# Kernel tuning notes

Measured on AMD Instinct MI355X. Metric: run time of the kernel, lower is better.

## Reference

```python
import jax, jax.numpy as jnp
import numpy as np

B, T, D, S = 4, 8192, 512, 16

def setup_inputs() -> dict:
    key = jax.random.key(0)
    k1, k2, k3, k4, k5 = jax.random.split(key, 5)
    x = jax.random.normal(k1, (B, T, D), dtype=jnp.float32)
    # splat parameters as in __init__: centers ~ 0.02*randn, log_scales = 0
    centers = jax.random.normal(k2, (S, D), dtype=jnp.float32) * 0.02
    log_scales = jnp.zeros((S,), dtype=jnp.float32)
    # xavier-uniform linear weights (gain = 1/(1+layer_idx*0.1) = 1.0 for layer 0)
    limit = float(np.sqrt(6.0 / (D + D)))
    Wv = jax.random.uniform(k3, (D, D), minval=-limit, maxval=limit, dtype=jnp.float32)
    Wo = jax.random.uniform(k4, (D, D), minval=-limit, maxval=limit, dtype=jnp.float32)
    return {"x": x, "centers": centers, "log_scales": log_scales, "Wv": Wv, "Wo": Wo}

def reference(x, centers, log_scales, Wv, Wo):
    # scales clamped as in EnhancedAdaptiveSplat.get_scale
    scales = jnp.clip(jnp.exp(log_scales), 0.1, 2.0)           # [S]
    v = jnp.einsum('btd,ed->bte', x, Wv)                       # value projection [B,T,D]
    # squared distance token<->splat via expansion (no [B,T,S,D] intermediate)
    x2 = jnp.sum(x * x, axis=-1, keepdims=True)                # [B,T,1]
    c2 = jnp.sum(centers * centers, axis=-1)                   # [S]
    xc = jnp.einsum('btd,sd->bts', x, centers)                 # [B,T,S]
    d2 = x2 + c2 - 2.0 * xc                                    # [B,T,S]
    logits = -0.5 * d2 / (scales * scales)                     # gaussian kernel log-weights
    attn = jax.nn.softmax(logits, axis=-1)                     # normalize over splats [B,T,S]
    # tokens -> splats aggregation, then splats -> tokens distribution
    splat_states = jnp.einsum('bts,btd->bsd', attn, v)         # [B,S,D]
    out = jnp.einsum('bts,bsd->btd', attn, splat_states)       # [B,T,D]
    return jnp.einsum('btd,ed->bte', out, Wo)                  # output projection
```

## Files before the change

### kernel.cpp

```cpp
#include <hip/hip_runtime.h>
#include <hip/hip_bf16.h>
#include <math.h>

#define B_ 4
#define T_ 8192
#define D_ 512
#define S_ 16

#define CHUNK 64


typedef __attribute__((ext_vector_type(8))) short bf16x8;
typedef __attribute__((ext_vector_type(4))) float f32x4;

__device__ __forceinline__ float dot4(float4 a, float4 b) {
  return a.x * b.x + a.y * b.y + a.z * b.z + a.w * b.w;
}

__device__ __forceinline__ bf16x8 pack8(float4 a, float4 b) {
  union { __hip_bfloat162 h[4]; bf16x8 v; } u;
  u.h[0] = __float22bfloat162_rn(make_float2(a.x, a.y));
  u.h[1] = __float22bfloat162_rn(make_float2(a.z, a.w));
  u.h[2] = __float22bfloat162_rn(make_float2(b.x, b.y));
  u.h[3] = __float22bfloat162_rn(make_float2(b.z, b.w));
  return u.v;
}

__global__ __launch_bounds__(256, 2) void attn_ts_k(const float* __restrict__ x,
                                                    const float* __restrict__ centers,
                                                    const float* __restrict__ log_scales,
                                                    float* __restrict__ attn,
                                                    float* __restrict__ ts) {
  __shared__ __align__(16) float a_s[CHUNK][S_];
  __shared__ __align__(16) bf16x8 cf_s[16][64];
  __shared__ float c2_s[S_];
  const int tid = threadIdx.x;
  const int lane = tid & 63;
  const int w = tid >> 6;
  const int g = lane >> 4;
  const int n = lane & 15;
  const int b = blockIdx.x >> 7;
  const int t0 = (blockIdx.x & 127) * CHUNK;
  const int tw = t0 + (w << 4);

#pragma unroll
  for (int i = 0; i < 4; ++i) {
    int e = i * 256 + tid;
    int st = e >> 6;
    int ln = e & 63;
    int nn = ln & 15, gg = ln >> 4;
    const float* src = centers + nn * D_ + st * 32 + (gg << 3);
    float4 c0 = *(const float4*)(src);
    float4 c1 = *(const float4*)(src + 4);
    cf_s[st][ln] = pack8(c0, c1);
  }
  if (w == 0) {
    const float* crow = centers + n * D_ + (g << 7);
    float c2p = 0.f;
#pragma unroll
    for (int k = 0; k < 32; ++k) {
      float4 cv = *(const float4*)(crow + (k << 2));
      c2p += dot4(cv, cv);
    }
    c2p += __shfl_xor(c2p, 16, 64);
    c2p += __shfl_xor(c2p, 32, 64);
    if (lane < S_) c2_s[lane] = c2p;
  }
  __syncthreads();

  {
    const float sc = fminf(fmaxf(__expf(log_scales[n]), 0.1f), 2.0f);
    const float inv2 = 0.5f / (sc * sc);
    const bool uni =
        (__ballot(sc == __shfl(sc, 0, 64)) == 0xFFFFFFFFFFFFFFFFull);

    const float* xrow = x + ((size_t)b * T_ + tw + n) * D_ + (g << 3);
    f32x4 acc = {0.f, 0.f, 0.f, 0.f};
    float x2p = 0.f;

    float4 pb0[4], pb1[4];
#pragma unroll
    for (int i = 0; i < 4; ++i) {
      pb0[i] = *(const float4*)(xrow + i * 32);
      pb1[i] = *(const float4*)(xrow + i * 32 + 4);
    }

    if (uni) {
#pragma unroll
      for (int st = 0; st < 16; ++st) {
        float4 x0 = pb0[st & 3], x1 = pb1[st & 3];
        if (st < 12) {
          pb0[st & 3] = *(const float4*)(xrow + (st + 4) * 32);
          pb1[st & 3] = *(const float4*)(xrow + (st + 4) * 32 + 4);
        }
        acc = __builtin_amdgcn_mfma_f32_16x16x32_bf16(pack8(x0, x1),
                                                      cf_s[st][lane], acc,
                                                      0, 0, 0);
      }
    } else {
#pragma unroll
      for (int st = 0; st < 16; ++st) {
        float4 x0 = pb0[st & 3], x1 = pb1[st & 3];
        if (st < 12) {
          pb0[st & 3] = *(const float4*)(xrow + (st + 4) * 32);
          pb1[st & 3] = *(const float4*)(xrow + (st + 4) * 32 + 4);
        }
        x2p += dot4(x0, x0) + dot4(x1, x1);
        acc = __builtin_amdgcn_mfma_f32_16x16x32_bf16(pack8(x0, x1),
                                                      cf_s[st][lane], acc,
                                                      0, 0, 0);
      }
      x2p += __shfl_xor(x2p, 16, 64);
      x2p += __shfl_xor(x2p, 32, 64);
    }

    const float c2 = c2_s[n];

    float lg[4];
#pragma unroll
    for (int r = 0; r < 4; ++r) {
      float t = 2.f * acc[r] - c2;
      if (!uni) t -= __shfl(x2p, (lane & 48) | ((g << 2) + r), 64);
      lg[r] = t * inv2;
    }

    float mx[4] = {lg[0], lg[1], lg[2], lg[3]};
#pragma unroll
    for (int dlt = 1; dlt < 16; dlt <<= 1)
#pragma unroll
      for (int r = 0; r < 4; ++r) mx[r] = fmaxf(mx[r], __shfl_xor(mx[r], dlt, 64));
    float ev[4], sm[4];
#pragma unroll
    for (int r = 0; r < 4; ++r) { ev[r] = __expf(lg[r] - mx[r]); sm[r] = ev[r]; }
#pragma unroll
    for (int dlt = 1; dlt < 16; dlt <<= 1)
#pragma unroll
      for (int r = 0; r < 4; ++r) sm[r] += __shfl_xor(sm[r], dlt, 64);

    float* ar = attn + ((size_t)b * T_ + tw) * S_;
#pragma unroll
    for (int r = 0; r < 4; ++r) {
      float av = ev[r] / sm[r];
      int trow = (g << 2) + r;
      ar[trow * S_ + n] = av;
      a_s[(w << 4) + trow][n] = av;
    }
  }

  __syncthreads();

  {
    const int d = tid;
    float2 acc[S_];
#pragma unroll
    for (int si = 0; si < S_; ++si) acc[si] = make_float2(0.f, 0.f);

    const float* xb = x + ((size_t)b * T_ + t0) * D_;

#pragma unroll 8
    for (int t = 0; t < CHUNK; ++t) {
      float xv0 = xb[(size_t)t * D_ + d];
      float xv1 = xb[(size_t)t * D_ + d + 256];
      const float4* ap = (const float4*)a_s[t];
      float4 q0 = ap[0], q1 = ap[1], q2 = ap[2], q3 = ap[3];
      float av[S_] = {q0.x, q0.y, q0.z, q0.w, q1.x, q1.y, q1.z, q1.w,
                      q2.x, q2.y, q2.z, q2.w, q3.x, q3.y, q3.z, q3.w};
#pragma unroll
      for (int si = 0; si < S_; ++si) {
        acc[si].x += av[si] * xv0;
        acc[si].y += av[si] * xv1;
      }
    }

    float* tb = ts + (size_t)b * S_ * D_;
#pragma unroll
    for (int si = 0; si < S_; ++si) {
      atomicAdd(tb + si * D_ + d, acc[si].x);
      atomicAdd(tb + si * D_ + d + 256, acc[si].y);
    }
  }
}

__global__ __launch_bounds__(256) void proj_k(const float* __restrict__ in,
                                              const float* __restrict__ W,
                                              float* __restrict__ out) {
  __shared__ float red[4][64];
  const int r = blockIdx.x >> 3;
  const int eb = blockIdx.x & 7;
  const int el = threadIdx.x & 63;
  const int kc = threadIdx.x >> 6;
  const int e = (eb << 6) + el;

  const float4* w4 = (const float4*)(W + (size_t)e * D_ + kc * 128);
  const float4* i4 = (const float4*)(in + (size_t)r * D_ + kc * 128);
  float acc = 0.f;
#pragma unroll
  for (int k = 0; k < 32; ++k) acc += dot4(w4[k], i4[k]);

  red[kc][el] = acc;
  __syncthreads();
  if (kc == 0)
    out[(size_t)r * D_ + e] = red[0][el] + red[1][el] + red[2][el] + red[3][el];
}

#define K4_TOK 64
__global__ __launch_bounds__(256) void out_k(const float* __restrict__ attn,
                                             const float* __restrict__ ss_o,
                                             float* __restrict__ out) {
  const int chunks = T_ / K4_TOK;
  const int b = blockIdx.x / chunks;
  const int t0 = (blockIdx.x % chunks) * K4_TOK;
  const int w = threadIdx.x >> 6;
  const int lane = threadIdx.x & 63;
  const int e0 = (w << 7) + (lane << 1);

  float2 ssf[S_];
  const float* sb = ss_o + (size_t)b * S_ * D_;
#pragma unroll
  for (int s = 0; s < S_; ++s) ssf[s] = *(const float2*)(sb + s * D_ + e0);

  const float4* ab = (const float4*)(attn + ((size_t)b * T_ + t0) * S_);
  float* ob = out + ((size_t)b * T_ + t0) * D_ + e0;

#pragma unroll 4
  for (int t = 0; t < K4_TOK; ++t) {
    float4 a0 = ab[t * 4 + 0], a1 = ab[t * 4 + 1];
    float4 a2 = ab[t * 4 + 2], a3 = ab[t * 4 + 3];
    float av[S_] = {a0.x, a0.y, a0.z, a0.w, a1.x, a1.y, a1.z, a1.w,
                    a2.x, a2.y, a2.z, a2.w, a3.x, a3.y, a3.z, a3.w};
    float2 acc = make_float2(0.f, 0.f);
#pragma unroll
    for (int s = 0; s < S_; ++s) {
      acc.x += av[s] * ssf[s].x;
      acc.y += av[s] * ssf[s].y;
    }
    *(float2*)(ob + (size_t)t * D_) = acc;
  }
}

extern "C" void kernel_launch(void* const* d_in, const int* in_sizes, int n_in,
                              void* d_out, int out_size, void* d_ws, size_t ws_size,
                              hipStream_t stream) {
  const float* x          = (const float*)d_in[0];
  const float* centers    = (const float*)d_in[1];
  const float* log_scales = (const float*)d_in[2];
  const float* Wv         = (const float*)d_in[3];
  const float* Wo         = (const float*)d_in[4];
  float* out = (float*)d_out;

  float* attn = (float*)d_ws;
  float* ts   = attn + (size_t)B_ * T_ * S_;
  float* tmp  = ts + (size_t)B_ * S_ * D_;
  float* ss_o = tmp + (size_t)B_ * S_ * D_;

  hipMemsetAsync(ts, 0, (size_t)B_ * S_ * D_ * sizeof(float), stream);

  attn_ts_k<<<B_ * (T_ / CHUNK), 256, 0, stream>>>(x, centers, log_scales, attn, ts);
  proj_k<<<512, 256, 0, stream>>>(ts, Wv, tmp);
  proj_k<<<512, 256, 0, stream>>>(tmp, Wo, ss_o);
  out_k<<<B_ * (T_ / K4_TOK), 256, 0, stream>>>(attn, ss_o, out);
}
```

Baseline: 177.5 us.

## Compute output distribution with bf16 MFMA instead of scalar FMA loop

The final kernel that multiplies attention weights by projected splat states now stages splat states into shared memory as bf16 and runs a 16x16x32 bf16 MFMA per 16-column tile, zero-padding the K dimension from 16 to 32. This moves the FP32 scalar FMA work onto matrix cores. The stores change to 4 scalar writes per lane with 16-wide column groups instead of float2 rows, which may be less coalesced. Precision drops to bf16 for attn and splat states.

```diff
diff --git a/kernel.cpp b/kernel.cpp
--- a/kernel.cpp
+++ b/kernel.cpp
@@ -203,38 +203,48 @@
     out[(size_t)r * D_ + e] = red[0][el] + red[1][el] + red[2][el] + red[3][el];
 }
 
-#define K4_TOK 64
 __global__ __launch_bounds__(256) void out_k(const float* __restrict__ attn,
                                              const float* __restrict__ ss_o,
                                              float* __restrict__ out) {
-  const int chunks = T_ / K4_TOK;
-  const int b = blockIdx.x / chunks;
-  const int t0 = (blockIdx.x % chunks) * K4_TOK;
-  const int w = threadIdx.x >> 6;
-  const int lane = threadIdx.x & 63;
-  const int e0 = (w << 7) + (lane << 1);
-
-  float2 ssf[S_];
-  const float* sb = ss_o + (size_t)b * S_ * D_;
-#pragma unroll
-  for (int s = 0; s < S_; ++s) ssf[s] = *(const float2*)(sb + s * D_ + e0);
-
-  const float4* ab = (const float4*)(attn + ((size_t)b * T_ + t0) * S_);
-  float* ob = out + ((size_t)b * T_ + t0) * D_ + e0;
-
+  __shared__ __align__(16) __hip_bfloat16 bs[32][16][16];
+  const int tid = threadIdx.x;
+  const int lane = tid & 63;
+  const int w = tid >> 6;
+  const int g = lane >> 4;
+  const int n = lane & 15;
+  const int b = blockIdx.x >> 7;
+  const int t0 = (blockIdx.x & 127) * 64;
+  const int tw = t0 + (w << 4);
+
+  {
+    const float* sb = ss_o + (size_t)b * S_ * D_;
+    const int e0 = tid, e1 = tid + 256;
+#pragma unroll
+    for (int s = 0; s < S_; ++s) {
+      bs[e0 >> 4][e0 & 15][s] = __float2bfloat16(sb[s * D_ + e0]);
+      bs[e1 >> 4][e1 & 15][s] = __float2bfloat16(sb[s * D_ + e1]);
+    }
+  }
+  __syncthreads();
+
+  bf16x8 af = {0, 0, 0, 0, 0, 0, 0, 0};
+  {
+    const float* arow = attn + ((size_t)b * T_ + tw + n) * S_ + ((g & 1) << 3);
+    float4 a0 = *(const float4*)(arow);
+    float4 a1 = *(const float4*)(arow + 4);
+    bf16x8 full = pack8(a0, a1);
+    if (g < 2) af = full;
+  }
+
+  float* ob = out + ((size_t)b * T_ + tw) * D_;
 #pragma unroll 4
-  for (int t = 0; t < K4_TOK; ++t) {
-    float4 a0 = ab[t * 4 + 0], a1 = ab[t * 4 + 1];
-    float4 a2 = ab[t * 4 + 2], a3 = ab[t * 4 + 3];
-    float av[S_] = {a0.x, a0.y, a0.z, a0.w, a1.x, a1.y, a1.z, a1.w,
-                    a2.x, a2.y, a2.z, a2.w, a3.x, a3.y, a3.z, a3.w};
-    float2 acc = make_float2(0.f, 0.f);
-#pragma unroll
-    for (int s = 0; s < S_; ++s) {
-      acc.x += av[s] * ssf[s].x;
-      acc.y += av[s] * ssf[s].y;
-    }
-    *(float2*)(ob + (size_t)t * D_) = acc;
+  for (int et = 0; et < 32; ++et) {
+    bf16x8 bfr = *(const bf16x8*)&bs[et][n][(g & 1) << 3];
+    f32x4 z = {0.f, 0.f, 0.f, 0.f};
+    f32x4 d = __builtin_amdgcn_mfma_f32_16x16x32_bf16(af, bfr, z, 0, 0, 0);
+    float* oc = ob + et * 16 + n;
+#pragma unroll
+    for (int r = 0; r < 4; ++r) oc[(size_t)((g << 2) + r) * D_] = d[r];
   }
 }
 
@@ -258,5 +268,5 @@
   attn_ts_k<<<B_ * (T_ / CHUNK), 256, 0, stream>>>(x, centers, log_scales, attn, ts);
   proj_k<<<512, 256, 0, stream>>>(ts, Wv, tmp);
   proj_k<<<512, 256, 0, stream>>>(tmp, Wo, ss_o);
-  out_k<<<B_ * (T_ / K4_TOK), 256, 0, stream>>>(attn, ss_o, out);
-}
+  out_k<<<512, 256, 0, stream>>>(attn, ss_o, out);
+}
```

New measurement: 170.2 us. -4.1%, faster.
